# Kernel optimization log

Hardware: AMD Instinct MI355X
Metric: run time of the kernel (lower is better)

Reference implementation:

```python
import jax, jax.numpy as jnp
import numpy as np

B, T, U, D = 8, 200, 50, 512
INNER, VOCAB = 640, 1024


def setup_inputs() -> dict:
    key = jax.random.key(0)
    k1, k2, k3, k4 = jax.random.split(key, 4)
    enc_outputs = jax.random.normal(k1, (B, T, D), dtype=jnp.float32)
    dec_outputs = jax.random.normal(k2, (B, U, D), dtype=jnp.float32)
    # Dense(inner_dim, activation='tanh') params
    W1 = jax.random.normal(k3, (D, INNER), dtype=jnp.float32) / np.sqrt(D)
    b1 = jnp.zeros((INNER,), dtype=jnp.float32)
    # Dense(vocab_size) params
    W2 = jax.random.normal(k4, (INNER, VOCAB), dtype=jnp.float32) / np.sqrt(INNER)
    b2 = jnp.zeros((VOCAB,), dtype=jnp.float32)
    return {"enc_outputs": enc_outputs, "dec_outputs": dec_outputs,
            "W1": W1, "b1": b1, "W2": W2, "b2": b2}


def reference(enc_outputs, dec_outputs, W1, b1, W2, b2):
    # joint_inputs: (B, T, U, D) via broadcast add, exactly as the TF module
    joint = enc_outputs[:, :, None, :] + dec_outputs[:, None, :, :]
    hidden = jnp.tanh(jnp.einsum('btud,dh->btuh', joint, W1) + b1)  # (B,T,U,INNER)
    logits = jnp.einsum('btuh,hv->btuv', hidden, W2) + b2            # (B,T,U,VOCAB)
    return logits
```

## Files before the change

kernel.cpp:

```cpp
#include <hip/hip_runtime.h>
#include <hip/hip_bf16.h>
#include <stdint.h>

namespace {

constexpr int B = 8, T = 200, U = 50, D = 512, INNER = 640, VOCAB = 1024;
constexpr int M_TOTAL = B * T * U;
constexpr int ROWS_E = B * T;
constexpr int ROWS_D = B * U;
constexpr int ROWS_ED = ROWS_E + ROWS_D;
constexpr int BM = 64;
constexpr int KST = INNER / 32;

typedef __bf16 bf16x8 __attribute__((ext_vector_type(8)));
typedef float  f32x4  __attribute__((ext_vector_type(4)));
typedef unsigned short u16;
typedef unsigned int   u32;

__device__ __forceinline__ u16 f2bf(float f) {
  uint32_t u = __float_as_uint(f);
  uint32_t rounding = 0x7FFFu + ((u >> 16) & 1u);
  return (u16)((u + rounding) >> 16);
}

__device__ __forceinline__ float fast_tanh(float x) {
  float e = __expf(2.0f * x);
  float r = __builtin_amdgcn_rcpf(e + 1.0f);
  return 1.0f - 2.0f * r;
}

__global__ __launch_bounds__(320) void k_prep(const float* __restrict__ enc,
                                              const float* __restrict__ dec,
                                              const float* __restrict__ W1,
                                              const float* __restrict__ b1,
                                              const float* __restrict__ W2,
                                              float* __restrict__ ED,
                                              u16* __restrict__ W2B) {
  if (blockIdx.x >= 250) {
    const int idx = (blockIdx.x - 250) * 320 + threadIdx.x;
    const int lane = idx & 63;
    const int f = idx >> 6;
    const int ks = f >> 6;
    const int nf = f & 63;
    const int n = nf * 16 + (lane & 15);
    const int k = ks * 32 + (lane >> 4) * 8;
    u16 v[8];
#pragma unroll
    for (int j = 0; j < 8; ++j)
      v[j] = f2bf(W2[(size_t)(k + j) * VOCAB + n]);
    uint64_t lo = (uint64_t)v[0] | ((uint64_t)v[1] << 16) |
                  ((uint64_t)v[2] << 32) | ((uint64_t)v[3] << 48);
    uint64_t hi = (uint64_t)v[4] | ((uint64_t)v[5] << 16) |
                  ((uint64_t)v[6] << 32) | ((uint64_t)v[7] << 48);
    uint64_t* dst = reinterpret_cast<uint64_t*>(W2B + (size_t)idx * 8);
    dst[0] = lo;
    dst[1] = hi;
    return;
  }

  __shared__ float rows[8 * D];
  const int r0 = blockIdx.x * 8;
  const bool is_enc = (r0 < ROWS_E);
  const float* src = is_enc ? (enc + (size_t)r0 * D)
                            : (dec + (size_t)(r0 - ROWS_E) * D);
  for (int i = threadIdx.x; i < 8 * D; i += 320) rows[i] = src[i];
  __syncthreads();

  const int c0 = threadIdx.x, c1 = threadIdx.x + 320;
  float acc[8][2];
  const float bias0 = is_enc ? b1[c0] : 0.f;
  const float bias1 = is_enc ? b1[c1] : 0.f;
#pragma unroll
  for (int r = 0; r < 8; ++r) { acc[r][0] = bias0; acc[r][1] = bias1; }

  for (int d = 0; d < D; d += 4) {
    float4 rv[8];
#pragma unroll
    for (int r = 0; r < 8; ++r)
      rv[r] = *reinterpret_cast<const float4*>(&rows[r * D + d]);
#pragma unroll
    for (int dd = 0; dd < 4; ++dd) {
      const float w0 = W1[(size_t)(d + dd) * INNER + c0];
      const float w1 = W1[(size_t)(d + dd) * INNER + c1];
#pragma unroll
      for (int r = 0; r < 8; ++r) {
        const float x = (dd == 0) ? rv[r].x : (dd == 1) ? rv[r].y
                        : (dd == 2) ? rv[r].z : rv[r].w;
        acc[r][0] = fmaf(x, w0, acc[r][0]);
        acc[r][1] = fmaf(x, w1, acc[r][1]);
      }
    }
  }
#pragma unroll
  for (int r = 0; r < 8; ++r) {
    ED[(size_t)(r0 + r) * INNER + c0] = acc[r][0];
    ED[(size_t)(r0 + r) * INNER + c1] = acc[r][1];
  }
}

__global__ __launch_bounds__(1024, 4) void k_main(const float* __restrict__ ED,
                                                  const u16* __restrict__ W2B,
                                                  const float* __restrict__ b2,
                                                  float* __restrict__ out) {
  __shared__ u16 At[BM * INNER];
  char* At_b = reinterpret_cast<char*>(At);

  const int tid = threadIdx.x;
  const int m0 = blockIdx.x * BM;

#pragma unroll
  for (int i = 0; i < 5; ++i) {
    const int c = i * 1024 + tid;
    const int row = c / 80;
    const int kc = (c - row * 80) * 8;
    const int m = m0 + row;
    const int b = m / (T * U);
    const int rem = m - b * (T * U);
    const int t = rem / U;
    const int u = rem - t * U;
    const float* Erow = ED + (size_t)(b * T + t) * INNER + kc;
    const float* Drow = ED + (size_t)(ROWS_E + b * U + u) * INNER + kc;
    const float4 e0 = *reinterpret_cast<const float4*>(Erow);
    const float4 e1 = *reinterpret_cast<const float4*>(Erow + 4);
    const float4 d0 = *reinterpret_cast<const float4*>(Drow);
    const float4 d1 = *reinterpret_cast<const float4*>(Drow + 4);
    const u32 p0 = (u32)f2bf(fast_tanh(e0.x + d0.x)) |
                   ((u32)f2bf(fast_tanh(e0.y + d0.y)) << 16);
    const u32 p1 = (u32)f2bf(fast_tanh(e0.z + d0.z)) |
                   ((u32)f2bf(fast_tanh(e0.w + d0.w)) << 16);
    const u32 p2 = (u32)f2bf(fast_tanh(e1.x + d1.x)) |
                   ((u32)f2bf(fast_tanh(e1.y + d1.y)) << 16);
    const u32 p3 = (u32)f2bf(fast_tanh(e1.z + d1.z)) |
                   ((u32)f2bf(fast_tanh(e1.w + d1.w)) << 16);
    const int byte = (row * (INNER * 2) + kc * 2) ^ ((row & 7) << 4);
    int4 pk; pk.x = (int)p0; pk.y = (int)p1; pk.z = (int)p2; pk.w = (int)p3;
    *reinterpret_cast<int4*>(At_b + byte) = pk;
  }
  __syncthreads();

  const int lane = tid & 63;
  const int w    = tid >> 6;
  const int llo  = lane & 15;
  const int lhi  = lane >> 4;

  int abase[4];
  const int aswz = (llo & 7) << 4;
#pragma unroll
  for (int mi = 0; mi < 4; ++mi)
    abase[mi] = (mi * 16 + llo) * (INNER * 2) + lhi * 16;

  const u16* Bp = W2B + ((size_t)(w * 4) * 512 + (size_t)lane * 8);

  f32x4 acc[4][4];
#pragma unroll
  for (int mi = 0; mi < 4; ++mi)
#pragma unroll
    for (int ni = 0; ni < 4; ++ni) acc[mi][ni] = (f32x4){0.f, 0.f, 0.f, 0.f};

#pragma unroll 2
  for (int ks = 0; ks < KST; ++ks) {
    bf16x8 a[4];
#pragma unroll
    for (int mi = 0; mi < 4; ++mi)
      a[mi] = *reinterpret_cast<const bf16x8*>(At_b + ((abase[mi] + ks * 64) ^ aswz));
    bf16x8 bfr[4];
#pragma unroll
    for (int ni = 0; ni < 4; ++ni)
      bfr[ni] = *reinterpret_cast<const bf16x8*>(Bp + (size_t)ks * 32768 + ni * 512);
#pragma unroll
    for (int mi = 0; mi < 4; ++mi)
#pragma unroll
      for (int ni = 0; ni < 4; ++ni)
        acc[mi][ni] = __builtin_amdgcn_mfma_f32_16x16x32_bf16(a[mi], bfr[ni], acc[mi][ni], 0, 0, 0);
  }

  float b2v[4];
#pragma unroll
  for (int ni = 0; ni < 4; ++ni) b2v[ni] = b2[w * 64 + ni * 16 + llo];

#pragma unroll
  for (int mi = 0; mi < 4; ++mi) {
#pragma unroll
    for (int q = 0; q < 4; ++q) {
      const int row = m0 + mi * 16 + lhi * 4 + q;
      float* orow = out + (size_t)row * VOCAB + w * 64 + llo;
#pragma unroll
      for (int ni = 0; ni < 4; ++ni)
        orow[ni * 16] = acc[mi][ni][q] + b2v[ni];
    }
  }
}

}

extern "C" void kernel_launch(void* const* d_in, const int* in_sizes, int n_in,
                              void* d_out, int out_size, void* d_ws, size_t ws_size,
                              hipStream_t stream) {
  const float* enc = (const float*)d_in[0];
  const float* dec = (const float*)d_in[1];
  const float* W1  = (const float*)d_in[2];
  const float* b1  = (const float*)d_in[3];
  const float* W2  = (const float*)d_in[4];
  const float* b2  = (const float*)d_in[5];
  float* out = (float*)d_out;

  float* ED  = (float*)d_ws;
  u16*   W2B = (u16*)((char*)d_ws + (size_t)ROWS_ED * INNER * 4);

  hipLaunchKernelGGL(k_prep, dim3(506), dim3(320), 0, stream,
                     enc, dec, W1, b1, W2, ED, W2B);
  hipLaunchKernelGGL(k_main, dim3(M_TOTAL / BM), dim3(1024), 0, stream,
                     ED, W2B, b2, out);
}
```

Before: 191.6 us.

## Double-buffer tanh A-tile in K-chunks and split vocab across grid y

The main GEMM kernel now uses 128-row by 512-column tiles with 512 threads and a second grid dimension over the vocabulary. The tanh hidden tile is built in four K-chunks into a double-buffered LDS layout in MFMA fragment order, so each chunk's tanh production overlaps the MFMAs on the previous chunk. B fragments are software-prefetched one k-step ahead. This targets the serial tanh-then-GEMM phase and the LDS swizzle cost. In exchange the tanh work is done twice (once per vocab half), there are more registers per thread (32 accumulators), and block-level syncs are added per chunk.

```diff
diff --git a/kernel.cpp b/kernel.cpp
--- a/kernel.cpp
+++ b/kernel.cpp
@@ -9,8 +9,9 @@
 constexpr int ROWS_E = B * T;
 constexpr int ROWS_D = B * U;
 constexpr int ROWS_ED = ROWS_E + ROWS_D;
-constexpr int BM = 64;
-constexpr int KST = INNER / 32;
+constexpr int BM = 128, BN = 512;
+constexpr int BKC = 160;
+constexpr int CHUNK_LDS = (BM / 16) * 5 * 1024;
 
 typedef __bf16 bf16x8 __attribute__((ext_vector_type(8)));
 typedef float  f32x4  __attribute__((ext_vector_type(4)));
@@ -98,97 +99,124 @@
   }
 }
 
-__global__ __launch_bounds__(1024, 4) void k_main(const float* __restrict__ ED,
-                                                  const u16* __restrict__ W2B,
-                                                  const float* __restrict__ b2,
-                                                  float* __restrict__ out) {
-  __shared__ u16 At[BM * INNER];
+__global__ __launch_bounds__(512, 2) void k_main(const float* __restrict__ ED,
+                                                 const u16* __restrict__ W2B,
+                                                 const float* __restrict__ b2,
+                                                 float* __restrict__ out) {
+  __shared__ u16 At[2 * CHUNK_LDS / 2];
   char* At_b = reinterpret_cast<char*>(At);
 
   const int tid = threadIdx.x;
   const int m0 = blockIdx.x * BM;
-
-#pragma unroll
-  for (int i = 0; i < 5; ++i) {
-    const int c = i * 1024 + tid;
-    const int row = c / 80;
-    const int kc = (c - row * 80) * 8;
-    const int m = m0 + row;
-    const int b = m / (T * U);
-    const int rem = m - b * (T * U);
-    const int t = rem / U;
-    const int u = rem - t * U;
-    const float* Erow = ED + (size_t)(b * T + t) * INNER + kc;
-    const float* Drow = ED + (size_t)(ROWS_E + b * U + u) * INNER + kc;
-    const float4 e0 = *reinterpret_cast<const float4*>(Erow);
-    const float4 e1 = *reinterpret_cast<const float4*>(Erow + 4);
-    const float4 d0 = *reinterpret_cast<const float4*>(Drow);
-    const float4 d1 = *reinterpret_cast<const float4*>(Drow + 4);
-    const u32 p0 = (u32)f2bf(fast_tanh(e0.x + d0.x)) |
-                   ((u32)f2bf(fast_tanh(e0.y + d0.y)) << 16);
-    const u32 p1 = (u32)f2bf(fast_tanh(e0.z + d0.z)) |
-                   ((u32)f2bf(fast_tanh(e0.w + d0.w)) << 16);
-    const u32 p2 = (u32)f2bf(fast_tanh(e1.x + d1.x)) |
-                   ((u32)f2bf(fast_tanh(e1.y + d1.y)) << 16);
-    const u32 p3 = (u32)f2bf(fast_tanh(e1.z + d1.z)) |
-                   ((u32)f2bf(fast_tanh(e1.w + d1.w)) << 16);
-    const int byte = (row * (INNER * 2) + kc * 2) ^ ((row & 7) << 4);
-    int4 pk; pk.x = (int)p0; pk.y = (int)p1; pk.z = (int)p2; pk.w = (int)p3;
-    *reinterpret_cast<int4*>(At_b + byte) = pk;
-  }
-  __syncthreads();
+  const int n0 = blockIdx.y * BN;
+
+  const int wrow = tid >> 2;
+  const int wj   = tid & 3;
+  {
+  }
+  const int m = m0 + wrow;
+  const int bb = m / (T * U);
+  const int rem = m - bb * (T * U);
+  const int tt = rem / U;
+  const int uu = rem - tt * U;
+  const float* Erow = ED + (size_t)(bb * T + tt) * INNER;
+  const float* Drow = ED + (size_t)(ROWS_E + bb * U + uu) * INNER;
+  const int wlds = ((wrow >> 4) * 5) * 1024 + (wj * 16 + (wrow & 15)) * 16;
+
+#define TANH_CHUNK(cc, buf)                                                    \
+  {                                                                            \
+    const int kb = (cc) * BKC;                                                 \
+    _Pragma("unroll")                                                          \
+    for (int i = 0; i < 5; ++i) {                                              \
+      const int kk = kb + (i * 4 + wj) * 8;                                    \
+      const float4 e0 = *reinterpret_cast<const float4*>(Erow + kk);           \
+      const float4 e1 = *reinterpret_cast<const float4*>(Erow + kk + 4);       \
+      const float4 d0 = *reinterpret_cast<const float4*>(Drow + kk);           \
+      const float4 d1 = *reinterpret_cast<const float4*>(Drow + kk + 4);       \
+      const u32 p0 = (u32)f2bf(fast_tanh(e0.x + d0.x)) |                       \
+                     ((u32)f2bf(fast_tanh(e0.y + d0.y)) << 16);                \
+      const u32 p1 = (u32)f2bf(fast_tanh(e0.z + d0.z)) |                       \
+                     ((u32)f2bf(fast_tanh(e0.w + d0.w)) << 16);                \
+      const u32 p2 = (u32)f2bf(fast_tanh(e1.x + d1.x)) |                       \
+                     ((u32)f2bf(fast_tanh(e1.y + d1.y)) << 16);                \
+      const u32 p3 = (u32)f2bf(fast_tanh(e1.z + d1.z)) |                       \
+                     ((u32)f2bf(fast_tanh(e1.w + d1.w)) << 16);                \
+      int4 pk; pk.x = (int)p0; pk.y = (int)p1; pk.z = (int)p2; pk.w = (int)p3; \
+      *reinterpret_cast<int4*>(At_b + (buf) * 40960 + wlds + i * 1024) = pk;   \
+    }                                                                          \
+  }
 
   const int lane = tid & 63;
   const int w    = tid >> 6;
   const int llo  = lane & 15;
   const int lhi  = lane >> 4;
-
-  int abase[4];
-  const int aswz = (llo & 7) << 4;
-#pragma unroll
-  for (int mi = 0; mi < 4; ++mi)
-    abase[mi] = (mi * 16 + llo) * (INNER * 2) + lhi * 16;
-
-  const u16* Bp = W2B + ((size_t)(w * 4) * 512 + (size_t)lane * 8);
-
-  f32x4 acc[4][4];
-#pragma unroll
-  for (int mi = 0; mi < 4; ++mi)
+  const int lane16 = lane * 16;
+
+  const u16* Bp = W2B + ((size_t)(n0 / 16 + w * 4) << 9) + lane * 8;
+
+  f32x4 acc[8][4];
+#pragma unroll
+  for (int mi = 0; mi < 8; ++mi)
 #pragma unroll
     for (int ni = 0; ni < 4; ++ni) acc[mi][ni] = (f32x4){0.f, 0.f, 0.f, 0.f};
 
-#pragma unroll 2
-  for (int ks = 0; ks < KST; ++ks) {
-    bf16x8 a[4];
-#pragma unroll
-    for (int mi = 0; mi < 4; ++mi)
-      a[mi] = *reinterpret_cast<const bf16x8*>(At_b + ((abase[mi] + ks * 64) ^ aswz));
-    bf16x8 bfr[4];
+  TANH_CHUNK(0, 0)
+  __syncthreads();
+
+#pragma unroll
+  for (int c = 0; c < 4; ++c) {
+    const int abase = (c & 1) * 40960;
+
+    bf16x8 bcur[4];
 #pragma unroll
     for (int ni = 0; ni < 4; ++ni)
-      bfr[ni] = *reinterpret_cast<const bf16x8*>(Bp + (size_t)ks * 32768 + ni * 512);
-#pragma unroll
-    for (int mi = 0; mi < 4; ++mi)
-#pragma unroll
-      for (int ni = 0; ni < 4; ++ni)
-        acc[mi][ni] = __builtin_amdgcn_mfma_f32_16x16x32_bf16(a[mi], bfr[ni], acc[mi][ni], 0, 0, 0);
+      bcur[ni] = *reinterpret_cast<const bf16x8*>(Bp + (((size_t)(c * 5) * 64 + ni) << 9));
+
+    if (c < 3) TANH_CHUNK(c + 1, (c + 1) & 1)
+
+#pragma unroll
+    for (int ks = 0; ks < 5; ++ks) {
+      bf16x8 bnext[4];
+      if (ks < 4) {
+#pragma unroll
+        for (int ni = 0; ni < 4; ++ni)
+          bnext[ni] = *reinterpret_cast<const bf16x8*>(
+              Bp + (((size_t)(c * 5 + ks + 1) * 64 + ni) << 9));
+      }
+      bf16x8 a[8];
+#pragma unroll
+      for (int mi = 0; mi < 8; ++mi)
+        a[mi] = *reinterpret_cast<const bf16x8*>(
+            At_b + abase + (mi * 5 + ks) * 1024 + lane16);
+#pragma unroll
+      for (int mi = 0; mi < 8; ++mi)
+#pragma unroll
+        for (int ni = 0; ni < 4; ++ni)
+          acc[mi][ni] = __builtin_amdgcn_mfma_f32_16x16x32_bf16(a[mi], bcur[ni], acc[mi][ni], 0, 0, 0);
+      if (ks < 4) {
+#pragma unroll
+        for (int ni = 0; ni < 4; ++ni) bcur[ni] = bnext[ni];
+      }
+    }
+    __syncthreads();
   }
 
   float b2v[4];
 #pragma unroll
-  for (int ni = 0; ni < 4; ++ni) b2v[ni] = b2[w * 64 + ni * 16 + llo];
-
-#pragma unroll
-  for (int mi = 0; mi < 4; ++mi) {
+  for (int ni = 0; ni < 4; ++ni) b2v[ni] = b2[n0 + w * 64 + ni * 16 + llo];
+
+#pragma unroll
+  for (int mi = 0; mi < 8; ++mi) {
 #pragma unroll
     for (int q = 0; q < 4; ++q) {
       const int row = m0 + mi * 16 + lhi * 4 + q;
-      float* orow = out + (size_t)row * VOCAB + w * 64 + llo;
+      float* orow = out + (size_t)row * VOCAB + n0 + w * 64 + llo;
 #pragma unroll
       for (int ni = 0; ni < 4; ++ni)
         orow[ni * 16] = acc[mi][ni][q] + b2v[ni];
     }
   }
+#undef TANH_CHUNK
 }
 
 }
@@ -209,6 +237,6 @@
 
   hipLaunchKernelGGL(k_prep, dim3(506), dim3(320), 0, stream,
                      enc, dec, W1, b1, W2, ED, W2B);
-  hipLaunchKernelGGL(k_main, dim3(M_TOTAL / BM), dim3(1024), 0, stream,
+  hipLaunchKernelGGL(k_main, dim3(M_TOTAL / BM, VOCAB / BN), dim3(512), 0, stream,
                      ED, W2B, b2, out);
 }
```

Measured after the change: 242.2 us. 26.4% more time.

## Double-buffer tanh A-tiles over K chunks and split vocab across blocks

Applied to the files above, without the earlier changes.

The main kernel now splits the vocab dimension into two 512-wide column blocks with 512 threads each. It also stages the tanh/bf16 A operand in 128-wide K chunks, double-buffered in shared memory, so the tanh computation for the next chunk overlaps the MFMAs on the current one. This cuts LDS use from 80KB to 32KB per block, which allows more resident blocks, at the cost of computing tanh twice per row (once per column block). The prep kernel uses 4 rows per block for more parallelism, and output stores become nontemporal.

```diff
diff --git a/kernel.cpp b/kernel.cpp
--- a/kernel.cpp
+++ b/kernel.cpp
@@ -9,8 +9,10 @@
 constexpr int ROWS_E = B * T;
 constexpr int ROWS_D = B * U;
 constexpr int ROWS_ED = ROWS_E + ROWS_D;
-constexpr int BM = 64;
-constexpr int KST = INNER / 32;
+constexpr int BM = 64, BN = 512;
+constexpr int CK = 128;
+constexpr int NCHUNK = INNER / CK;
+constexpr int CHUNK_B = 16 * 1024;
 
 typedef __bf16 bf16x8 __attribute__((ext_vector_type(8)));
 typedef float  f32x4  __attribute__((ext_vector_type(4)));
@@ -36,8 +38,8 @@
                                               const float* __restrict__ W2,
                                               float* __restrict__ ED,
                                               u16* __restrict__ W2B) {
-  if (blockIdx.x >= 250) {
-    const int idx = (blockIdx.x - 250) * 320 + threadIdx.x;
+  if (blockIdx.x >= 500) {
+    const int idx = (blockIdx.x - 500) * 320 + threadIdx.x;
     const int lane = idx & 63;
     const int f = idx >> 6;
     const int ks = f >> 6;
@@ -58,135 +60,149 @@
     return;
   }
 
-  __shared__ float rows[8 * D];
-  const int r0 = blockIdx.x * 8;
+  __shared__ float rows[4 * D];
+  const int r0 = blockIdx.x * 4;
   const bool is_enc = (r0 < ROWS_E);
   const float* src = is_enc ? (enc + (size_t)r0 * D)
                             : (dec + (size_t)(r0 - ROWS_E) * D);
-  for (int i = threadIdx.x; i < 8 * D; i += 320) rows[i] = src[i];
+  for (int i = threadIdx.x; i < 4 * D; i += 320) rows[i] = src[i];
   __syncthreads();
 
   const int c0 = threadIdx.x, c1 = threadIdx.x + 320;
-  float acc[8][2];
+  float acc[4][2];
   const float bias0 = is_enc ? b1[c0] : 0.f;
   const float bias1 = is_enc ? b1[c1] : 0.f;
 #pragma unroll
-  for (int r = 0; r < 8; ++r) { acc[r][0] = bias0; acc[r][1] = bias1; }
-
-  for (int d = 0; d < D; d += 4) {
-    float4 rv[8];
-#pragma unroll
-    for (int r = 0; r < 8; ++r)
-      rv[r] = *reinterpret_cast<const float4*>(&rows[r * D + d]);
-#pragma unroll
-    for (int dd = 0; dd < 4; ++dd) {
+  for (int r = 0; r < 4; ++r) { acc[r][0] = bias0; acc[r][1] = bias1; }
+
+  for (int d = 0; d < D; d += 8) {
+    f32x4 rv[4][2];
+#pragma unroll
+    for (int r = 0; r < 4; ++r) {
+      rv[r][0] = *reinterpret_cast<const f32x4*>(&rows[r * D + d]);
+      rv[r][1] = *reinterpret_cast<const f32x4*>(&rows[r * D + d + 4]);
+    }
+#pragma unroll
+    for (int dd = 0; dd < 8; ++dd) {
       const float w0 = W1[(size_t)(d + dd) * INNER + c0];
       const float w1 = W1[(size_t)(d + dd) * INNER + c1];
 #pragma unroll
-      for (int r = 0; r < 8; ++r) {
-        const float x = (dd == 0) ? rv[r].x : (dd == 1) ? rv[r].y
-                        : (dd == 2) ? rv[r].z : rv[r].w;
+      for (int r = 0; r < 4; ++r) {
+        const float x = rv[r][dd >> 2][dd & 3];
         acc[r][0] = fmaf(x, w0, acc[r][0]);
         acc[r][1] = fmaf(x, w1, acc[r][1]);
       }
     }
   }
 #pragma unroll
-  for (int r = 0; r < 8; ++r) {
+  for (int r = 0; r < 4; ++r) {
     ED[(size_t)(r0 + r) * INNER + c0] = acc[r][0];
     ED[(size_t)(r0 + r) * INNER + c1] = acc[r][1];
   }
 }
 
-__global__ __launch_bounds__(1024, 4) void k_main(const float* __restrict__ ED,
-                                                  const u16* __restrict__ W2B,
-                                                  const float* __restrict__ b2,
-                                                  float* __restrict__ out) {
-  __shared__ u16 At[BM * INNER];
+__global__ __launch_bounds__(512, 4) void k_main(const float* __restrict__ ED,
+                                                 const u16* __restrict__ W2B,
+                                                 const float* __restrict__ b2,
+                                                 float* __restrict__ out) {
+  __shared__ u16 At[2 * CHUNK_B / 2];
   char* At_b = reinterpret_cast<char*>(At);
 
   const int tid = threadIdx.x;
   const int m0 = blockIdx.x * BM;
-
-#pragma unroll
-  for (int i = 0; i < 5; ++i) {
-    const int c = i * 1024 + tid;
-    const int row = c / 80;
-    const int kc = (c - row * 80) * 8;
+  const int n0 = blockIdx.y * BN;
+
+  const int row0 = tid >> 4;
+  const int g    = tid & 15;
+  int eoff[2], doff[2], wbyte[2];
+#pragma unroll
+  for (int i = 0; i < 2; ++i) {
+    const int row = row0 + i * 32;
     const int m = m0 + row;
     const int b = m / (T * U);
     const int rem = m - b * (T * U);
     const int t = rem / U;
     const int u = rem - t * U;
-    const float* Erow = ED + (size_t)(b * T + t) * INNER + kc;
-    const float* Drow = ED + (size_t)(ROWS_E + b * U + u) * INNER + kc;
-    const float4 e0 = *reinterpret_cast<const float4*>(Erow);
-    const float4 e1 = *reinterpret_cast<const float4*>(Erow + 4);
-    const float4 d0 = *reinterpret_cast<const float4*>(Drow);
-    const float4 d1 = *reinterpret_cast<const float4*>(Drow + 4);
-    const u32 p0 = (u32)f2bf(fast_tanh(e0.x + d0.x)) |
-                   ((u32)f2bf(fast_tanh(e0.y + d0.y)) << 16);
-    const u32 p1 = (u32)f2bf(fast_tanh(e0.z + d0.z)) |
-                   ((u32)f2bf(fast_tanh(e0.w + d0.w)) << 16);
-    const u32 p2 = (u32)f2bf(fast_tanh(e1.x + d1.x)) |
-                   ((u32)f2bf(fast_tanh(e1.y + d1.y)) << 16);
-    const u32 p3 = (u32)f2bf(fast_tanh(e1.z + d1.z)) |
-                   ((u32)f2bf(fast_tanh(e1.w + d1.w)) << 16);
-    const int byte = (row * (INNER * 2) + kc * 2) ^ ((row & 7) << 4);
-    int4 pk; pk.x = (int)p0; pk.y = (int)p1; pk.z = (int)p2; pk.w = (int)p3;
-    *reinterpret_cast<int4*>(At_b + byte) = pk;
-  }
-  __syncthreads();
+    eoff[i] = (b * T + t) * INNER;
+    doff[i] = (ROWS_E + b * U + u) * INNER;
+    wbyte[i] = (((row >> 4) * 4 + (g >> 2)) << 10) + ((g & 3) * 16 + (row & 15)) * 16;
+  }
+
+  auto tanh_chunk = [&](int c, int bufsel) __attribute__((always_inline)) {
+    const int kb = c * CK + g * 8;
+#pragma unroll
+    for (int i = 0; i < 2; ++i) {
+      const float* E = ED + eoff[i] + kb;
+      const float* Dp = ED + doff[i] + kb;
+      const f32x4 e0 = *reinterpret_cast<const f32x4*>(E);
+      const f32x4 e1 = *reinterpret_cast<const f32x4*>(E + 4);
+      const f32x4 d0 = *reinterpret_cast<const f32x4*>(Dp);
+      const f32x4 d1 = *reinterpret_cast<const f32x4*>(Dp + 4);
+      const u32 p0 = (u32)f2bf(fast_tanh(e0[0] + d0[0])) |
+                     ((u32)f2bf(fast_tanh(e0[1] + d0[1])) << 16);
+      const u32 p1 = (u32)f2bf(fast_tanh(e0[2] + d0[2])) |
+                     ((u32)f2bf(fast_tanh(e0[3] + d0[3])) << 16);
+      const u32 p2 = (u32)f2bf(fast_tanh(e1[0] + d1[0])) |
+                     ((u32)f2bf(fast_tanh(e1[1] + d1[1])) << 16);
+      const u32 p3 = (u32)f2bf(fast_tanh(e1[2] + d1[2])) |
+                     ((u32)f2bf(fast_tanh(e1[3] + d1[3])) << 16);
+      int4 pk; pk.x = (int)p0; pk.y = (int)p1; pk.z = (int)p2; pk.w = (int)p3;
+      *reinterpret_cast<int4*>(At_b + bufsel * CHUNK_B + wbyte[i]) = pk;
+    }
+  };
 
   const int lane = tid & 63;
   const int w    = tid >> 6;
   const int llo  = lane & 15;
   const int lhi  = lane >> 4;
-
-  int abase[4];
-  const int aswz = (llo & 7) << 4;
+  const u16* Bp = W2B + ((size_t)((n0 >> 4) + w * 4) << 9) + lane * 8;
+
+  f32x4 acc[4][4];
 #pragma unroll
   for (int mi = 0; mi < 4; ++mi)
-    abase[mi] = (mi * 16 + llo) * (INNER * 2) + lhi * 16;
-
-  const u16* Bp = W2B + ((size_t)(w * 4) * 512 + (size_t)lane * 8);
-
-  f32x4 acc[4][4];
-#pragma unroll
-  for (int mi = 0; mi < 4; ++mi)
 #pragma unroll
     for (int ni = 0; ni < 4; ++ni) acc[mi][ni] = (f32x4){0.f, 0.f, 0.f, 0.f};
 
-#pragma unroll 2
-  for (int ks = 0; ks < KST; ++ks) {
-    bf16x8 a[4];
-#pragma unroll
-    for (int mi = 0; mi < 4; ++mi)
-      a[mi] = *reinterpret_cast<const bf16x8*>(At_b + ((abase[mi] + ks * 64) ^ aswz));
-    bf16x8 bfr[4];
-#pragma unroll
-    for (int ni = 0; ni < 4; ++ni)
-      bfr[ni] = *reinterpret_cast<const bf16x8*>(Bp + (size_t)ks * 32768 + ni * 512);
-#pragma unroll
-    for (int mi = 0; mi < 4; ++mi)
+  tanh_chunk(0, 0);
+  __syncthreads();
+
+  for (int c = 0; c < NCHUNK; ++c) {
+    const int ab = (c & 1) * CHUNK_B;
+    if (c < NCHUNK - 1) tanh_chunk(c + 1, (c + 1) & 1);
+
+#pragma unroll
+    for (int ks = 0; ks < 4; ++ks) {
+      bf16x8 bfr[4], a[4];
 #pragma unroll
       for (int ni = 0; ni < 4; ++ni)
-        acc[mi][ni] = __builtin_amdgcn_mfma_f32_16x16x32_bf16(a[mi], bfr[ni], acc[mi][ni], 0, 0, 0);
+        bfr[ni] = *reinterpret_cast<const bf16x8*>(
+            Bp + ((size_t)((c * 4 + ks) * 64 + ni) << 9));
+#pragma unroll
+      for (int mi = 0; mi < 4; ++mi)
+        a[mi] = *reinterpret_cast<const bf16x8*>(
+            At_b + ab + ((mi * 4 + ks) << 10) + lane * 16);
+#pragma unroll
+      for (int mi = 0; mi < 4; ++mi)
+#pragma unroll
+        for (int ni = 0; ni < 4; ++ni)
+          acc[mi][ni] = __builtin_amdgcn_mfma_f32_16x16x32_bf16(a[mi], bfr[ni], acc[mi][ni], 0, 0, 0);
+    }
+    __syncthreads();
   }
 
   float b2v[4];
 #pragma unroll
-  for (int ni = 0; ni < 4; ++ni) b2v[ni] = b2[w * 64 + ni * 16 + llo];
+  for (int ni = 0; ni < 4; ++ni) b2v[ni] = b2[n0 + w * 64 + ni * 16 + llo];
 
 #pragma unroll
   for (int mi = 0; mi < 4; ++mi) {
 #pragma unroll
     for (int q = 0; q < 4; ++q) {
       const int row = m0 + mi * 16 + lhi * 4 + q;
-      float* orow = out + (size_t)row * VOCAB + w * 64 + llo;
+      float* orow = out + (size_t)row * VOCAB + n0 + w * 64 + llo;
 #pragma unroll
       for (int ni = 0; ni < 4; ++ni)
-        orow[ni * 16] = acc[mi][ni][q] + b2v[ni];
+        __builtin_nontemporal_store(acc[mi][ni][q] + b2v[ni], orow + ni * 16);
     }
   }
 }
@@ -207,8 +223,8 @@
   float* ED  = (float*)d_ws;
   u16*   W2B = (u16*)((char*)d_ws + (size_t)ROWS_ED * INNER * 4);
 
-  hipLaunchKernelGGL(k_prep, dim3(506), dim3(320), 0, stream,
+  hipLaunchKernelGGL(k_prep, dim3(756), dim3(320), 0, stream,
                      enc, dec, W1, b1, W2, ED, W2B);
-  hipLaunchKernelGGL(k_main, dim3(M_TOTAL / BM), dim3(1024), 0, stream,
+  hipLaunchKernelGGL(k_main, dim3(M_TOTAL / BM, VOCAB / BN), dim3(512), 0, stream,
                      ED, W2B, b2, out);
 }
```

New measurement: 178.6 us. 1.07x faster.
